# Performance work log

Measured on AMD Instinct MI355X. Metric: run time of the kernel, lower is better.

The kernel has to match this reference:

```python
import jax, jax.numpy as jnp
import numpy as np

HEADS, DIM_HEAD, BITS = 12, 64, 4


def quantize(q, bits):
    # per-tensor affine fake-quant, exactly as the torch quantize()
    s = (q.max() - q.min()) / (2.0 ** bits - 1.0)
    z = jnp.round(2.0 ** bits - 1.0 - q.max() / s)
    return jnp.round(q / s + z), s, z


def setup_inputs() -> dict:
    key = jax.random.key(0)
    k1, k2, k3, k4 = jax.random.split(key, 4)
    return {
        "x": jax.random.normal(k1, (4, 1024, 768), jnp.float32),
        "w_qkv": jax.random.normal(k2, (2304, 768), jnp.float32) * 0.02,  # torch Linear weight [out,in]
        "w_out": jax.random.normal(k3, (768, 768), jnp.float32) * 0.02,
        "b_out": jax.random.normal(k4, (768,), jnp.float32) * 0.02,
    }


def reference(x, w_qkv, w_out, b_out):
    scale = DIM_HEAD ** -0.5
    B, N, D = x.shape
    # --- quantized QKV projection: x @ W^T with zero-point correction ---
    xq, sx1, zx1 = quantize(x, BITS)
    w1, sw1, zw1 = quantize(w_qkv.T, BITS)  # [D, 3*inner]
    xqkv = (xq @ w1
            - w1.sum(0, keepdims=True) * zx1
            - xq.sum(2, keepdims=True) * zw1
            + zx1 * zw1 * D) * (sx1 * sw1)  # [B, N, 3*inner]
    q, k, v = jnp.split(xqkv, 3, axis=-1)
    to_heads = lambda t: t.reshape(B, N, HEADS, DIM_HEAD).transpose(0, 2, 1, 3)  # b h n d
    q, k, v = to_heads(q), to_heads(k), to_heads(v)
    # --- quantized QK^T (note: original omits the +zq*zk*d term) ---
    qq, sq, zq = quantize(q, BITS)
    kq, sk, zk = quantize(k.transpose(0, 1, 3, 2), BITS)  # b h d n
    dots = (qq @ kq
            - kq.sum(2, keepdims=True) * zq
            - qq.sum(3, keepdims=True) * zk) * (scale * sq * sk)  # b h n n
    a = jax.nn.softmax(dots, axis=-1)
    # --- quantized A @ V ---
    aq, sa, za = quantize(a, BITS)
    vq, sv, zv = quantize(v, BITS)
    out = (aq @ vq
           - vq.sum(2, keepdims=True) * za
           - aq.sum(3, keepdims=True) * zv
           + za * zv * N) * (sa * sv)  # b h n d
    out = out.transpose(0, 2, 1, 3).reshape(B, N, HEADS * DIM_HEAD)
    # --- quantized output projection (faithful to original: correction uses
    # xqkv.sum / xqkv width, reproducing the source's use of `x` here) ---
    oq, sx2, zx2 = quantize(out, BITS)
    w2, sw2, zw2 = quantize(w_out.T, BITS)  # [inner, D]
    o = (oq @ w2
         - w2.sum(0, keepdims=True) * zx2
         - xqkv.sum(2, keepdims=True) * zw2
         + zx2 * zw2 * xqkv.shape[2]) * (sx2 * sw2) + b_out
    return o
```

## Files before the change

kernel.cpp:

```cpp
#include <hip/hip_runtime.h>
#include <math.h>

#define HEADS 12
#define DH    64
#define Dm    768
#define I3    2304
#define Nn    1024
#define Mm    4096
#define BHt   48
#define LOG2E 1.4426950408889634f

#define P_X  0
#define P_W1 1
#define P_Q  2
#define P_K  3
#define P_V  4
#define P_A  5
#define P_O  6
#define P_W2 7

typedef int v4i __attribute__((ext_vector_type(4)));

#if __has_builtin(__builtin_amdgcn_exp2f)
#define EXP2(x) __builtin_amdgcn_exp2f(x)
#else
#define EXP2(x) exp2f(x)
#endif

__device__ inline unsigned encf(float f) {
    unsigned u = __float_as_uint(f);
    return (u & 0x80000000u) ? ~u : (u | 0x80000000u);
}
__device__ inline float decf(unsigned u) {
    return (u & 0x80000000u) ? __uint_as_float(u & 0x7fffffffu) : __uint_as_float(~u);
}
__device__ inline void get_sz(const unsigned* scal, int pair, float* s, float* z) {
    float mn = decf(scal[2 * pair]);
    float mx = decf(scal[2 * pair + 1]);
    float ss = (mx - mn) / 15.0f;
    *s = ss;
    *z = rintf(15.0f - mx / ss);
}

__device__ inline void swz_bh(int blk, int* bh, int* itile) {
    int xcd = blk & 7, idx = blk >> 3;
    *itile = idx & 15;
    *bh = xcd + 8 * (idx >> 4);
}

__global__ __launch_bounds__(256) void k_init(unsigned* scal, float* z1, int n1, float* z2, int n2) {
    int g = blockIdx.x * 256 + threadIdx.x;
    if (g < n1) z1[g] = 0.f;
    if (g < n2) z2[g] = 0.f;
    if (g < 8) { scal[2 * g] = 0xFFFFFFFFu; scal[2 * g + 1] = 0u; }
}

__global__ __launch_bounds__(256) void k_minmax3(const float* x, const float* w1, const float* w2,
                                                 unsigned* scal) {
    __shared__ float rmn[256], rmx[256];
    int bid = blockIdx.x, tid = threadIdx.x;
    const float* src; int rows, pair, b0, nb;
    if (bid < 256)      { src = x;  rows = 4096; pair = P_X;  b0 = 0;   nb = 256; }
    else if (bid < 384) { src = w1; rows = 2304; pair = P_W1; b0 = 256; nb = 128; }
    else                { src = w2; rows = 768;  pair = P_W2; b0 = 384; nb = 64;  }
    float mn = INFINITY, mx = -INFINITY;
    for (int r = bid - b0; r < rows; r += nb) {
        const float* row = src + (long)r * 768;
#pragma unroll
        for (int k = 0; k < 3; ++k) {
            float v = row[tid + k * 256];
            mn = fminf(mn, v); mx = fmaxf(mx, v);
        }
    }
    rmn[tid] = mn; rmx[tid] = mx; __syncthreads();
    for (int s = 128; s > 0; s >>= 1) {
        if (tid < s) { rmn[tid] = fminf(rmn[tid], rmn[tid + s]); rmx[tid] = fmaxf(rmx[tid], rmx[tid + s]); }
        __syncthreads();
    }
    if (tid == 0) {
        atomicMin(&scal[2 * pair], encf(rmn[0]));
        atomicMax(&scal[2 * pair + 1], encf(rmx[0]));
    }
}

__global__ __launch_bounds__(256) void k_quant3(const float* x, const float* w1, const float* w2,
                                                const unsigned* scal,
                                                signed char* xq, signed char* wq, signed char* w2q,
                                                float* rs_x, float* rs_w1, float* rs_w2) {
    __shared__ float red[256];
    int bid = blockIdx.x, tid = threadIdx.x;
    const float* src; signed char* dq; float* rs; int pair, r;
    if (bid < 4096)      { src = x;  dq = xq;  rs = rs_x;  pair = P_X;  r = bid; }
    else if (bid < 6400) { src = w1; dq = wq;  rs = rs_w1; pair = P_W1; r = bid - 4096; }
    else                 { src = w2; dq = w2q; rs = rs_w2; pair = P_W2; r = bid - 6400; }
    float s, z; get_sz(scal, pair, &s, &z);
    const float* row = src + (long)r * 768;
    signed char* drow = dq + (long)r * 768;
    float acc = 0.f;
#pragma unroll
    for (int k = 0; k < 3; ++k) {
        int c = tid + k * 256;
        float q = rintf(row[c] / s + z);
        drow[c] = (signed char)(int)q;
        acc += q;
    }
    red[tid] = acc; __syncthreads();
    for (int s2 = 128; s2 > 0; s2 >>= 1) { if (tid < s2) red[tid] += red[tid + s2]; __syncthreads(); }
    if (tid == 0) rs[r] = red[0];
}

__global__ __launch_bounds__(256) void k_quant_rows(const float* src, const unsigned* scal, int pair,
                                                    signed char* dq) {
    int r = blockIdx.x, tid = threadIdx.x;
    float s, z; get_sz(scal, pair, &s, &z);
    const float* row = src + (long)r * 768;
    signed char* drow = dq + (long)r * 768;
#pragma unroll
    for (int k = 0; k < 3; ++k) {
        int c = tid + k * 256;
        float q = rintf(row[c] / s + z);
        drow[c] = (signed char)(int)q;
    }
}

__global__ __launch_bounds__(256) void k_gemm_mfma(const signed char* A, const signed char* B,
                                                   const float* colsumB, const float* rowsumA,
                                                   const float* bias, float* C, int K, int ldC,
                                                   const unsigned* scal, int pairA, int pairB,
                                                   float corrK, int do_stats, float* rowsum_out,
                                                   unsigned* scal_mm) {
    __shared__ __align__(16) signed char As[128 * 64];
    __shared__ __align__(16) signed char Bs[128 * 64];
    __shared__ float red[256];
    int tid = threadIdx.x;
    int wave = tid >> 6, lane = tid & 63;
    int col16 = lane & 15, quad = lane >> 4;
    long rowbase = (long)blockIdx.y * 128;
    long colbase = (long)blockIdx.x * 128;

    int c4 = tid & 3, r4 = tid >> 2;
    const signed char* ag0 = A + (rowbase + r4) * K + c4 * 16;
    const signed char* ag1 = A + (rowbase + r4 + 64) * K + c4 * 16;
    const signed char* bg0 = B + (colbase + r4) * K + c4 * 16;
    const signed char* bg1 = B + (colbase + r4 + 64) * K + c4 * 16;
    int soff0 = ((r4 >> 4) << 10) + (c4 << 8) + ((r4 & 15) << 4);
    int soff1 = soff0 + 4096;

    v4i ra0 = *(const v4i*)ag0;
    v4i ra1 = *(const v4i*)ag1;
    v4i rb0 = *(const v4i*)bg0;
    v4i rb1 = *(const v4i*)bg1;

    const int afrag_off = wave * 2048 + quad * 256 + col16 * 16;
    const int bfrag_off = quad * 256 + col16 * 16;
    v4i acc[2][8] = {};
    int nk = K >> 6;
    for (int kt = 0; kt < nk; ++kt) {
        *(v4i*)(As + soff0) = ra0;
        *(v4i*)(As + soff1) = ra1;
        *(v4i*)(Bs + soff0) = rb0;
        *(v4i*)(Bs + soff1) = rb1;
        __syncthreads();
        if (kt + 1 < nk) {
            int ko = (kt + 1) << 6;
            ra0 = *(const v4i*)(ag0 + ko);
            ra1 = *(const v4i*)(ag1 + ko);
            rb0 = *(const v4i*)(bg0 + ko);
            rb1 = *(const v4i*)(bg1 + ko);
        }
        v4i af0 = *(const v4i*)(As + afrag_off);
        v4i af1 = *(const v4i*)(As + afrag_off + 1024);
        v4i bf[8];
#pragma unroll
        for (int g = 0; g < 8; ++g) bf[g] = *(const v4i*)(Bs + bfrag_off + g * 1024);
#pragma unroll
        for (int g = 0; g < 8; ++g) {
            acc[0][g] = __builtin_amdgcn_mfma_i32_16x16x64_i8(af0, bf[g], acc[0][g], 0, 0, 0);
            acc[1][g] = __builtin_amdgcn_mfma_i32_16x16x64_i8(af1, bf[g], acc[1][g], 0, 0, 0);
        }
        __syncthreads();
    }

    float sA, zA, sB, zB;
    get_sz(scal, pairA, &sA, &zA);
    get_sz(scal, pairB, &sB, &zB);
    float sAB = sA * sB;
    float zz = (zA * zB) * corrK;
    float vmn = INFINITY, vmx = -INFINITY;
    float rowpart[2][4] = {};
#pragma unroll
    for (int i2 = 0; i2 < 2; ++i2)
#pragma unroll
        for (int g = 0; g < 8; ++g) {
            long col = colbase + g * 16 + col16;
            float cs = colsumB[col] * zA;
            float bv = bias ? bias[col] : 0.f;
#pragma unroll
            for (int r = 0; r < 4; ++r) {
                long row = rowbase + wave * 32 + i2 * 16 + quad * 4 + r;
                float v = ((float)acc[i2][g][r] - cs - rowsumA[row] * zB + zz) * sAB + bv;
                C[row * ldC + col] = v;
                rowpart[i2][r] += v;
                vmn = fminf(vmn, v); vmx = fmaxf(vmx, v);
            }
        }
    if (do_stats) {
#pragma unroll
        for (int i2 = 0; i2 < 2; ++i2)
#pragma unroll
            for (int r = 0; r < 4; ++r) {
                float s = rowpart[i2][r];
                s += __shfl_xor(s, 1); s += __shfl_xor(s, 2);
                s += __shfl_xor(s, 4); s += __shfl_xor(s, 8);
                if (col16 == 0)
                    atomicAdd(&rowsum_out[rowbase + wave * 32 + i2 * 16 + quad * 4 + r], s);
            }
        int pair = P_Q + (int)(colbase / 768);
        red[tid] = vmx; __syncthreads();
        for (int s = 128; s > 0; s >>= 1) { if (tid < s) red[tid] = fmaxf(red[tid], red[tid + s]); __syncthreads(); }
        if (tid == 0) atomicMax(&scal_mm[2 * pair + 1], encf(red[0]));
        __syncthreads();
        red[tid] = vmn; __syncthreads();
        for (int s = 128; s > 0; s >>= 1) { if (tid < s) red[tid] = fminf(red[tid], red[tid + s]); __syncthreads(); }
        if (tid == 0) atomicMin(&scal_mm[2 * pair], encf(red[0]));
    }
}

__global__ __launch_bounds__(256) void k_quant_qkv2(const float* xqkv, const unsigned* scal,
                                                    signed char* qq, signed char* kq, signed char* vqT,
                                                    float* rowsum_qq, float* cskc, float* colsum_vq) {
    __shared__ __align__(16) signed char vt[64 * 80];
    __shared__ float vred[4][64];
    int blk = blockIdx.x;
    int bh = blk >> 4, itile = blk & 15;
    int tid = threadIdx.x;
    int wave = tid >> 6, d = tid & 63;
    int b = bh / HEADS, h = bh - HEADS * b;
    float sq, zq, sk, zk, sv, zv;
    get_sz(scal, P_Q, &sq, &zq);
    get_sz(scal, P_K, &sk, &zk);
    get_sz(scal, P_V, &sv, &zv);
    float zqcsc2 = zq * ((0.125f * sq) * sk) * LOG2E;
    int vb = 0;
    float vsum = 0.f;
    for (int ir = 0; ir < 16; ++ir) {
        int il = wave * 16 + ir;
        int i = itile * 64 + il;
        const float* row = xqkv + ((long)b * Nn + i) * I3 + h * DH;
        float q = rintf(row[d] / sq + zq);
        float k = rintf(row[768 + d] / sk + zk);
        float v = rintf(row[1536 + d] / sv + zv);
        long o = ((long)bh * Nn + i) * 64 + d;
        qq[o] = (signed char)(int)q;
        kq[o] = (signed char)(int)k;
        vsum += v;
        vb |= ((int)v & 0xff) << ((ir & 3) * 8);
        if ((ir & 3) == 3) {
            *(int*)(vt + d * 80 + (il & ~3)) = vb;
            vb = 0;
        }
        float s1 = q, s2 = k;
        for (int off = 32; off > 0; off >>= 1) {
            s1 += __shfl_down(s1, off);
            s2 += __shfl_down(s2, off);
        }
        if (d == 0) { rowsum_qq[bh * Nn + i] = s1; cskc[bh * Nn + i] = s2 * zqcsc2; }
    }
    vred[wave][d] = vsum;
    __syncthreads();
    int dd = tid >> 2, c = tid & 3;
    *(v4i*)(vqT + ((long)bh * 64 + dd) * 1024 + itile * 64 + c * 16) = *(const v4i*)(vt + dd * 80 + c * 16);
    if (tid < 64)
        atomicAdd(&colsum_vq[bh * 64 + tid],
                  ((vred[0][tid] + vred[1][tid]) + vred[2][tid]) + vred[3][tid]);
}

__global__ __launch_bounds__(256) void k_attn_a8(const signed char* qq, const signed char* kq,
                                                 const float* rowsum_qq, const float* cskc,
                                                 unsigned* scal, float* rowmax, float* sumexp) {
    __shared__ float red[256];
    int bh, itile;
    swz_bh(blockIdx.x, &bh, &itile);
    int tid = threadIdx.x;
    int wave = tid >> 6, lane = tid & 63;
    int col16 = lane & 15, quad = lane >> 4;
    int rowbase = itile * 64 + wave * 16;
    const signed char* kbase = kq + (long)bh * Nn * 64;
    const float* ck = cskc + bh * Nn;
    v4i afrag = *(const v4i*)(qq + ((long)bh * Nn + rowbase + col16) * 64 + quad * 16);
    float sq, zq, sk, zk;
    get_sz(scal, P_Q, &sq, &zq);
    get_sz(scal, P_K, &sk, &zk);
    float csc2 = ((0.125f * sq) * sk) * LOG2E;
    float rzc[4];
#pragma unroll
    for (int r = 0; r < 4; ++r)
        rzc[r] = rowsum_qq[bh * Nn + rowbase + quad * 4 + r] * zk * csc2;
    v4i zero = {0, 0, 0, 0};
    float m[4]    = {-INFINITY, -INFINITY, -INFINITY, -INFINITY};
    float se[4]   = {0.f, 0.f, 0.f, 0.f};
    float lmin[4] = {INFINITY, INFINITY, INFINITY, INFINITY};
    const signed char* kf = kbase + (long)col16 * 64 + quad * 16;
    const float* ckp = ck + col16;
    v4i kb[2][4];
    float ckc[4], ckn[4];
#pragma unroll
    for (int t = 0; t < 4; ++t) {
        kb[0][t] = *(const v4i*)(kf + (long)(t * 16) * 64);
        ckc[t] = ckp[t * 16];
    }
#pragma unroll 2
    for (int ch = 0; ch < 16; ++ch) {
        int cur = ch & 1, nxt = cur ^ 1;
        int pch = (ch < 15) ? ch + 1 : 15;
#pragma unroll
        for (int t = 0; t < 4; ++t) {
            kb[nxt][t] = *(const v4i*)(kf + (long)(pch * 64 + t * 16) * 64);
            ckn[t] = ckp[pch * 64 + t * 16];
        }
#pragma unroll
        for (int t = 0; t < 4; ++t) {
            v4i d = __builtin_amdgcn_mfma_i32_16x16x64_i8(afrag, kb[cur][t], zero, 0, 0, 0);
            float ckv = ckc[t];
#pragma unroll
            for (int r = 0; r < 4; ++r) {
                float dv = fmaf((float)d[r], csc2, -(ckv + rzc[r]));
                lmin[r] = fminf(lmin[r], dv);
                float mn = fmaxf(m[r], dv);
                float e = EXP2(fminf(m[r], dv) - mn);
                se[r] = (dv > m[r]) ? fmaf(se[r], e, 1.0f) : (se[r] + e);
                m[r] = mn;
            }
        }
#pragma unroll
        for (int t = 0; t < 4; ++t) ckc[t] = ckn[t];
    }
#pragma unroll
    for (int r = 0; r < 4; ++r) {
#pragma unroll
        for (int off = 1; off < 16; off <<= 1) {
            float mo = __shfl_xor(m[r], off);
            float so = __shfl_xor(se[r], off);
            float mino = __shfl_xor(lmin[r], off);
            float mn = fmaxf(m[r], mo);
            se[r] = fmaf(se[r], EXP2(m[r] - mn), so * EXP2(mo - mn));
            m[r] = mn;
            lmin[r] = fminf(lmin[r], mino);
        }
    }
    float amax_c = -INFINITY, amin_c = INFINITY;
    if (col16 == 0) {
#pragma unroll
        for (int r = 0; r < 4; ++r) {
            int grow = bh * Nn + rowbase + quad * 4 + r;
            rowmax[grow] = m[r];
            sumexp[grow] = se[r];
            amax_c = fmaxf(amax_c, 1.0f / se[r]);
            amin_c = fminf(amin_c, EXP2(lmin[r] - m[r]) / se[r]);
        }
    }
    red[tid] = amax_c; __syncthreads();
    for (int s = 128; s > 0; s >>= 1) { if (tid < s) red[tid] = fmaxf(red[tid], red[tid + s]); __syncthreads(); }
    if (tid == 0) atomicMax(&scal[2 * P_A + 1], encf(red[0]));
    __syncthreads();
    red[tid] = amin_c; __syncthreads();
    for (int s = 128; s > 0; s >>= 1) { if (tid < s) red[tid] = fminf(red[tid], red[tid + s]); __syncthreads(); }
    if (tid == 0) atomicMin(&scal[2 * P_A], encf(red[0]));
}

__global__ __launch_bounds__(256) void k_attn_b8(const signed char* qq, const signed char* kq,
                                                 const signed char* vqT, const float* rowsum_qq,
                                                 const float* cskc, const float* colsum_vq,
                                                 const float* rowmax, const float* sumexp,
                                                 unsigned* scal, float* out_mat) {
    __shared__ __align__(16) signed char AqB[8192];
    __shared__ float red[256];
    int bh, itile;
    swz_bh(blockIdx.x, &bh, &itile);
    int tid = threadIdx.x;
    int wave = tid >> 6, lane = tid & 63;
    int col16 = lane & 15, quad = lane >> 4;
    int rowbase = itile * 64 + wave * 16;
    int b = bh / HEADS, h = bh - HEADS * b;
    const signed char* kbase = kq + (long)bh * Nn * 64;
    const signed char* vbase = vqT + (long)bh * 64 * 1024;
    const float* ck = cskc + bh * Nn;
    v4i afrag = *(const v4i*)(qq + ((long)bh * Nn + rowbase + col16) * 64 + quad * 16);
    float sq, zq, sk, zk, sv, zv, sa, za;
    get_sz(scal, P_Q, &sq, &zq);
    get_sz(scal, P_K, &sk, &zk);
    get_sz(scal, P_V, &sv, &zv);
    get_sz(scal, P_A, &sa, &za);
    float csc2 = ((0.125f * sq) * sk) * LOG2E;
    float roff[4], crcp[4];
#pragma unroll
    for (int r = 0; r < 4; ++r) {
        int row = bh * Nn + rowbase + quad * 4 + r;
        roff[r] = rowsum_qq[row] * zk * csc2 + rowmax[row];
        crcp[r] = 1.0f / (sumexp[row] * sa);
    }
    v4i accPV[4] = {};
    float rs_a[4] = {0.f, 0.f, 0.f, 0.f};
    v4i zero = {0, 0, 0, 0};
    const signed char* kf = kbase + (long)col16 * 64 + quad * 16;
    const float* ckp = ck + col16;
    const int pa_off = wave * 1024 + col16 * 64 + ((quad ^ (col16 >> 2)) << 4);

    v4i kb0[4], kb1[4];
    float ckr0[4], ckr1[4];
#pragma unroll
    for (int t = 0; t < 4; ++t) {
        kb0[t] = *(const v4i*)(kf + (long)(t * 16) * 64);
        ckr0[t] = ckp[t * 16];
        kb1[t] = *(const v4i*)(kf + (long)(64 + t * 16) * 64);
        ckr1[t] = ckp[64 + t * 16];
    }

#define QUANT_CHUNK(BUF, KB, CKR)                                                       \
    {                                                                                   \
        signed char* myAq = AqB + (BUF) * 4096 + wave * 1024;                           \
        _Pragma("unroll")                                                               \
        for (int t = 0; t < 4; ++t) {                                                   \
            v4i d = __builtin_amdgcn_mfma_i32_16x16x64_i8(afrag, KB[t], zero, 0, 0, 0); \
            float ckv = CKR[t];                                                         \
            int cswz = ((t ^ quad) << 4) + col16;                                       \
            _Pragma("unroll")                                                           \
            for (int r = 0; r < 4; ++r) {                                               \
                float es = fmaf((float)d[r], csc2, -(ckv + roff[r]));                   \
                float fastv = fmaf(EXP2(es), crcp[r], za);                              \
                float aqv = rintf(fastv);                                               \
                rs_a[r] += aqv;                                                         \
                myAq[(quad * 4 + r) * 64 + cswz] = (signed char)(int)aqv;               \
            }                                                                           \
        }                                                                               \
    }

#define BODY(CH, CUR, KBc, CKc, KBn, CKn)                                               \
    {                                                                                   \
        v4i pa = *(const v4i*)(AqB + (CUR) * 4096 + pa_off);                            \
        v4i bv[4];                                                                      \
        _Pragma("unroll")                                                               \
        for (int g = 0; g < 4; ++g)                                                     \
            bv[g] = *(const v4i*)(vbase + (long)(g * 16 + col16) * 1024 + (CH) * 64 + quad * 16); \
        if ((CH) < 14) {                                                                \
            _Pragma("unroll")                                                           \
            for (int t = 0; t < 4; ++t) {                                               \
                KBc[t] = *(const v4i*)(kf + (long)(((CH) + 2) * 64 + t * 16) * 64);     \
                CKc[t] = ckp[((CH) + 2) * 64 + t * 16];                                 \
            }                                                                           \
        }                                                                               \
        if ((CH) < 15) QUANT_CHUNK(1 - (CUR), KBn, CKn)                                 \
        _Pragma("unroll")                                                               \
        for (int g = 0; g < 4; ++g)                                                     \
            accPV[g] = __builtin_amdgcn_mfma_i32_16x16x64_i8(pa, bv[g], accPV[g], 0, 0, 0); \
    }

    QUANT_CHUNK(0, kb0, ckr0)
    for (int ch2 = 0; ch2 < 8; ++ch2) {
        int ch = ch2 * 2;
        BODY(ch, 0, kb0, ckr0, kb1, ckr1)
        BODY(ch + 1, 1, kb1, ckr1, kb0, ckr0)
    }
#undef BODY
#undef QUANT_CHUNK

#pragma unroll
    for (int r = 0; r < 4; ++r)
        for (int off = 1; off < 16; off <<= 1) rs_a[r] += __shfl_xor(rs_a[r], off);
    float sav = sa * sv;
    float zz = (za * zv) * 1024.0f;
    float vmn = INFINITY, vmx = -INFINITY;
#pragma unroll
    for (int g = 0; g < 4; ++g) {
        int d = g * 16 + col16;
        float cs = colsum_vq[bh * 64 + d] * za;
#pragma unroll
        for (int r = 0; r < 4; ++r) {
            int i = rowbase + quad * 4 + r;
            float v = ((float)accPV[g][r] - cs - rs_a[r] * zv + zz) * sav;
            out_mat[((long)b * Nn + i) * Dm + h * DH + d] = v;
            vmn = fminf(vmn, v); vmx = fmaxf(vmx, v);
        }
    }
    red[tid] = vmx; __syncthreads();
    for (int s = 128; s > 0; s >>= 1) { if (tid < s) red[tid] = fmaxf(red[tid], red[tid + s]); __syncthreads(); }
    if (tid == 0) atomicMax(&scal[2 * P_O + 1], encf(red[0]));
    __syncthreads();
    red[tid] = vmn; __syncthreads();
    for (int s = 128; s > 0; s >>= 1) { if (tid < s) red[tid] = fminf(red[tid], red[tid + s]); __syncthreads(); }
    if (tid == 0) atomicMin(&scal[2 * P_O], encf(red[0]));
}

extern "C" void kernel_launch(void* const* d_in, const int* in_sizes, int n_in,
                              void* d_out, int out_size, void* d_ws, size_t ws_size,
                              hipStream_t stream) {
    const float* x     = (const float*)d_in[0];
    const float* w_qkv = (const float*)d_in[1];
    const float* w_out = (const float*)d_in[2];
    const float* b_out = (const float*)d_in[3];

    char* ws = (char*)d_ws;
    size_t off = 0;
    auto alloc = [&](size_t n) -> char* {
        char* p = ws + off;
        off = (off + n + 255) & ~(size_t)255;
        return p;
    };
    unsigned*    scal        = (unsigned*)alloc(64);
    float*       xqkv        = (float*)alloc((size_t)Mm * I3 * 4);
    float*       out_mat     = (float*)alloc((size_t)Mm * Dm * 4);
    signed char* xq          = (signed char*)alloc((size_t)Mm * Dm);
    signed char* wq          = (signed char*)alloc((size_t)I3 * Dm);
    signed char* w2q         = (signed char*)alloc((size_t)Dm * Dm);
    signed char* oq          = (signed char*)alloc((size_t)Mm * Dm);
    signed char* qq          = (signed char*)alloc((size_t)BHt * Nn * DH);
    signed char* kq          = (signed char*)alloc((size_t)BHt * Nn * DH);
    signed char* vqT         = (signed char*)alloc((size_t)BHt * Nn * DH);
    float*       rowsum_xq   = (float*)alloc((size_t)Mm * 4);
    float*       colsum_w1   = (float*)alloc((size_t)I3 * 4);
    float*       colsum_w2   = (float*)alloc((size_t)Dm * 4);
    float*       rowsum_xqkv = (float*)alloc((size_t)Mm * 4);
    float*       rowsum_qq   = (float*)alloc((size_t)BHt * Nn * 4);
    float*       cskc        = (float*)alloc((size_t)BHt * Nn * 4);
    float*       colsum_vq   = (float*)alloc((size_t)BHt * DH * 4);
    float*       rowmax      = (float*)alloc((size_t)BHt * Nn * 4);
    float*       sumexp      = (float*)alloc((size_t)BHt * Nn * 4);

    k_init<<<28, 256, 0, stream>>>(scal, rowsum_xqkv, Mm, colsum_vq, BHt * DH);

    k_minmax3<<<448, 256, 0, stream>>>(x, w_qkv, w_out, scal);
    k_quant3<<<7168, 256, 0, stream>>>(x, w_qkv, w_out, scal, xq, wq, w2q,
                                       rowsum_xq, colsum_w1, colsum_w2);

    {
        dim3 g(I3 / 128, Mm / 128);
        k_gemm_mfma<<<g, 256, 0, stream>>>(xq, wq, colsum_w1, rowsum_xq, nullptr, xqkv,
                                           Dm, I3, scal, P_X, P_W1, 768.0f,
                                           1, rowsum_xqkv, scal);
    }

    k_quant_qkv2<<<BHt * 16, 256, 0, stream>>>(xqkv, scal, qq, kq, vqT,
                                               rowsum_qq, cskc, colsum_vq);

    k_attn_a8<<<BHt * 16, 256, 0, stream>>>(qq, kq, rowsum_qq, cskc, scal, rowmax, sumexp);
    k_attn_b8<<<BHt * 16, 256, 0, stream>>>(qq, kq, vqT, rowsum_qq, cskc, colsum_vq,
                                            rowmax, sumexp, scal, out_mat);

    k_quant_rows<<<Mm, 256, 0, stream>>>(out_mat, scal, P_O, oq);

    {
        dim3 g(Dm / 128, Mm / 128);
        k_gemm_mfma<<<g, 256, 0, stream>>>(oq, w2q, colsum_w2, rowsum_xqkv, b_out, (float*)d_out,
                                           Dm, Dm, scal, P_O, P_W2, 2304.0f,
                                           0, nullptr, nullptr);
    }
}
```

Before: 256.3 us.

## Transpose MFMA operands in attention kernels so each lane owns one query row

Swaps the A/B operand order of the int8 MFMA in both attention passes, so each lane's accumulator holds four key columns for a single query row rather than four rows. Row statistics (max, sum-exp, min, rowsum of quantized A) then reduce across 4 quads instead of 16 lanes. Column corrections become vectorized float4 loads. Quantized probabilities are packed into 32-bit LDS writes, and the output is written as float4. The aim is fewer shuffles, fewer scalar byte stores and loads, and fewer prefetch registers, at the cost of reworking the LDS layout for the PV operand.

```diff
diff --git a/kernel.cpp b/kernel.cpp
--- a/kernel.cpp
+++ b/kernel.cpp
@@ -19,7 +19,8 @@
 #define P_O  6
 #define P_W2 7
 
-typedef int v4i __attribute__((ext_vector_type(4)));
+typedef int   v4i __attribute__((ext_vector_type(4)));
+typedef float v4f __attribute__((ext_vector_type(4)));
 
 #if __has_builtin(__builtin_amdgcn_exp2f)
 #define EXP2(x) __builtin_amdgcn_exp2f(x)
@@ -286,45 +287,37 @@
     int col16 = lane & 15, quad = lane >> 4;
     int rowbase = itile * 64 + wave * 16;
     const signed char* kbase = kq + (long)bh * Nn * 64;
-    const float* ck = cskc + bh * Nn;
-    v4i afrag = *(const v4i*)(qq + ((long)bh * Nn + rowbase + col16) * 64 + quad * 16);
+    v4i qfrag = *(const v4i*)(qq + ((long)bh * Nn + rowbase + col16) * 64 + quad * 16);
     float sq, zq, sk, zk;
     get_sz(scal, P_Q, &sq, &zq);
     get_sz(scal, P_K, &sk, &zk);
     float csc2 = ((0.125f * sq) * sk) * LOG2E;
-    float rzc[4];
-#pragma unroll
-    for (int r = 0; r < 4; ++r)
-        rzc[r] = rowsum_qq[bh * Nn + rowbase + quad * 4 + r] * zk * csc2;
+    int irow = bh * Nn + rowbase + col16;
+    float roff = rowsum_qq[irow] * zk * csc2;
     v4i zero = {0, 0, 0, 0};
     float m[4]    = {-INFINITY, -INFINITY, -INFINITY, -INFINITY};
     float se[4]   = {0.f, 0.f, 0.f, 0.f};
     float lmin[4] = {INFINITY, INFINITY, INFINITY, INFINITY};
     const signed char* kf = kbase + (long)col16 * 64 + quad * 16;
-    const float* ckp = ck + col16;
+    const float* ckq = cskc + bh * Nn + quad * 4;
     v4i kb[2][4];
-    float ckc[4], ckn[4];
-#pragma unroll
-    for (int t = 0; t < 4; ++t) {
+#pragma unroll
+    for (int t = 0; t < 4; ++t)
         kb[0][t] = *(const v4i*)(kf + (long)(t * 16) * 64);
-        ckc[t] = ckp[t * 16];
-    }
 #pragma unroll 2
     for (int ch = 0; ch < 16; ++ch) {
         int cur = ch & 1, nxt = cur ^ 1;
         int pch = (ch < 15) ? ch + 1 : 15;
 #pragma unroll
-        for (int t = 0; t < 4; ++t) {
+        for (int t = 0; t < 4; ++t)
             kb[nxt][t] = *(const v4i*)(kf + (long)(pch * 64 + t * 16) * 64);
-            ckn[t] = ckp[pch * 64 + t * 16];
-        }
-#pragma unroll
-        for (int t = 0; t < 4; ++t) {
-            v4i d = __builtin_amdgcn_mfma_i32_16x16x64_i8(afrag, kb[cur][t], zero, 0, 0, 0);
-            float ckv = ckc[t];
+#pragma unroll
+        for (int s = 0; s < 4; ++s) {
+            v4i d = __builtin_amdgcn_mfma_i32_16x16x64_i8(kb[cur][s], qfrag, zero, 0, 0, 0);
+            v4f ck4 = *(const v4f*)(ckq + ch * 64 + s * 16);
 #pragma unroll
             for (int r = 0; r < 4; ++r) {
-                float dv = fmaf((float)d[r], csc2, -(ckv + rzc[r]));
+                float dv = fmaf((float)d[r], csc2, -(ck4[r] + roff));
                 lmin[r] = fminf(lmin[r], dv);
                 float mn = fmaxf(m[r], dv);
                 float e = EXP2(fminf(m[r], dv) - mn);
@@ -332,33 +325,28 @@
                 m[r] = mn;
             }
         }
-#pragma unroll
-        for (int t = 0; t < 4; ++t) ckc[t] = ckn[t];
-    }
-#pragma unroll
-    for (int r = 0; r < 4; ++r) {
-#pragma unroll
-        for (int off = 1; off < 16; off <<= 1) {
-            float mo = __shfl_xor(m[r], off);
-            float so = __shfl_xor(se[r], off);
-            float mino = __shfl_xor(lmin[r], off);
-            float mn = fmaxf(m[r], mo);
-            se[r] = fmaf(se[r], EXP2(m[r] - mn), so * EXP2(mo - mn));
-            m[r] = mn;
-            lmin[r] = fminf(lmin[r], mino);
-        }
-    }
-    float amax_c = -INFINITY, amin_c = INFINITY;
-    if (col16 == 0) {
-#pragma unroll
-        for (int r = 0; r < 4; ++r) {
-            int grow = bh * Nn + rowbase + quad * 4 + r;
-            rowmax[grow] = m[r];
-            sumexp[grow] = se[r];
-            amax_c = fmaxf(amax_c, 1.0f / se[r]);
-            amin_c = fminf(amin_c, EXP2(lmin[r] - m[r]) / se[r]);
-        }
-    }
+    }
+    float mm = fmaxf(fmaxf(m[0], m[1]), fmaxf(m[2], m[3]));
+    float seT = fmaf(se[0], EXP2(m[0] - mm),
+               fmaf(se[1], EXP2(m[1] - mm),
+               fmaf(se[2], EXP2(m[2] - mm), se[3] * EXP2(m[3] - mm))));
+    float lmT = fminf(fminf(lmin[0], lmin[1]), fminf(lmin[2], lmin[3]));
+#pragma unroll
+    for (int off = 16; off <= 32; off <<= 1) {
+        float mo = __shfl_xor(mm, off);
+        float so = __shfl_xor(seT, off);
+        float lo = __shfl_xor(lmT, off);
+        float mn = fmaxf(mm, mo);
+        seT = fmaf(seT, EXP2(mm - mn), so * EXP2(mo - mn));
+        mm = mn;
+        lmT = fminf(lmT, lo);
+    }
+    if (quad == 0) {
+        rowmax[irow] = mm;
+        sumexp[irow] = seT;
+    }
+    float amax_c = 1.0f / seT;
+    float amin_c = EXP2(lmT - mm) / seT;
     red[tid] = amax_c; __syncthreads();
     for (int s = 128; s > 0; s >>= 1) { if (tid < s) red[tid] = fmaxf(red[tid], red[tid + s]); __syncthreads(); }
     if (tid == 0) atomicMax(&scal[2 * P_A + 1], encf(red[0]));
@@ -384,103 +372,95 @@
     int b = bh / HEADS, h = bh - HEADS * b;
     const signed char* kbase = kq + (long)bh * Nn * 64;
     const signed char* vbase = vqT + (long)bh * 64 * 1024;
-    const float* ck = cskc + bh * Nn;
-    v4i afrag = *(const v4i*)(qq + ((long)bh * Nn + rowbase + col16) * 64 + quad * 16);
+    v4i qfrag = *(const v4i*)(qq + ((long)bh * Nn + rowbase + col16) * 64 + quad * 16);
     float sq, zq, sk, zk, sv, zv, sa, za;
     get_sz(scal, P_Q, &sq, &zq);
     get_sz(scal, P_K, &sk, &zk);
     get_sz(scal, P_V, &sv, &zv);
     get_sz(scal, P_A, &sa, &za);
     float csc2 = ((0.125f * sq) * sk) * LOG2E;
-    float roff[4], crcp[4];
-#pragma unroll
-    for (int r = 0; r < 4; ++r) {
-        int row = bh * Nn + rowbase + quad * 4 + r;
-        roff[r] = rowsum_qq[row] * zk * csc2 + rowmax[row];
-        crcp[r] = 1.0f / (sumexp[row] * sa);
-    }
+    int irow = bh * Nn + rowbase + col16;
+    float roff = rowsum_qq[irow] * zk * csc2 + rowmax[irow];
+    float crcp = 1.0f / (sumexp[irow] * sa);
     v4i accPV[4] = {};
-    float rs_a[4] = {0.f, 0.f, 0.f, 0.f};
+    float rs_a = 0.f;
     v4i zero = {0, 0, 0, 0};
     const signed char* kf = kbase + (long)col16 * 64 + quad * 16;
-    const float* ckp = ck + col16;
-    const int pa_off = wave * 1024 + col16 * 64 + ((quad ^ (col16 >> 2)) << 4);
+    const float* ckq = cskc + bh * Nn + quad * 4;
+    const int wbase = wave * 1024 + col16 * 16 + quad * 4;
+    const int rbase = wave * 1024 + quad * 256 + col16 * 16;
 
     v4i kb0[4], kb1[4];
-    float ckr0[4], ckr1[4];
 #pragma unroll
     for (int t = 0; t < 4; ++t) {
         kb0[t] = *(const v4i*)(kf + (long)(t * 16) * 64);
-        ckr0[t] = ckp[t * 16];
         kb1[t] = *(const v4i*)(kf + (long)(64 + t * 16) * 64);
-        ckr1[t] = ckp[64 + t * 16];
-    }
-
-#define QUANT_CHUNK(BUF, KB, CKR)                                                       \
+    }
+
+#define QUANT_CHUNK(CH, BUF, KB)                                                        \
     {                                                                                   \
-        signed char* myAq = AqB + (BUF) * 4096 + wave * 1024;                           \
         _Pragma("unroll")                                                               \
-        for (int t = 0; t < 4; ++t) {                                                   \
-            v4i d = __builtin_amdgcn_mfma_i32_16x16x64_i8(afrag, KB[t], zero, 0, 0, 0); \
-            float ckv = CKR[t];                                                         \
-            int cswz = ((t ^ quad) << 4) + col16;                                       \
+        for (int s = 0; s < 4; ++s) {                                                   \
+            v4i d = __builtin_amdgcn_mfma_i32_16x16x64_i8(KB[s], qfrag, zero, 0, 0, 0); \
+            v4f ck4 = *(const v4f*)(ckq + (CH) * 64 + s * 16);                          \
+            unsigned pks = 0;                                                           \
             _Pragma("unroll")                                                           \
             for (int r = 0; r < 4; ++r) {                                               \
-                float es = fmaf((float)d[r], csc2, -(ckv + roff[r]));                   \
-                float fastv = fmaf(EXP2(es), crcp[r], za);                              \
-                float aqv = rintf(fastv);                                               \
-                rs_a[r] += aqv;                                                         \
-                myAq[(quad * 4 + r) * 64 + cswz] = (signed char)(int)aqv;               \
+                float es = fmaf((float)d[r], csc2, -(ck4[r] + roff));                   \
+                float aqv = rintf(fmaf(EXP2(es), crcp, za));                            \
+                rs_a += aqv;                                                            \
+                pks |= ((unsigned)(int)aqv & 255u) << (8 * r);                          \
             }                                                                           \
+            *(int*)(AqB + (BUF) * 4096 + wbase + s * 256) = (int)pks;                   \
         }                                                                               \
     }
 
-#define BODY(CH, CUR, KBc, CKc, KBn, CKn)                                               \
+#define BODY(CH, CUR, KBc, KBn)                                                         \
     {                                                                                   \
-        v4i pa = *(const v4i*)(AqB + (CUR) * 4096 + pa_off);                            \
+        v4i pa = *(const v4i*)(AqB + (CUR) * 4096 + rbase);                             \
         v4i bv[4];                                                                      \
         _Pragma("unroll")                                                               \
         for (int g = 0; g < 4; ++g)                                                     \
             bv[g] = *(const v4i*)(vbase + (long)(g * 16 + col16) * 1024 + (CH) * 64 + quad * 16); \
         if ((CH) < 14) {                                                                \
             _Pragma("unroll")                                                           \
-            for (int t = 0; t < 4; ++t) {                                               \
+            for (int t = 0; t < 4; ++t)                                                 \
                 KBc[t] = *(const v4i*)(kf + (long)(((CH) + 2) * 64 + t * 16) * 64);     \
-                CKc[t] = ckp[((CH) + 2) * 64 + t * 16];                                 \
-            }                                                                           \
         }                                                                               \
-        if ((CH) < 15) QUANT_CHUNK(1 - (CUR), KBn, CKn)                                 \
+        if ((CH) < 15) QUANT_CHUNK((CH) + 1, 1 - (CUR), KBn)                            \
         _Pragma("unroll")                                                               \
         for (int g = 0; g < 4; ++g)                                                     \
-            accPV[g] = __builtin_amdgcn_mfma_i32_16x16x64_i8(pa, bv[g], accPV[g], 0, 0, 0); \
-    }
-
-    QUANT_CHUNK(0, kb0, ckr0)
+            accPV[g] = __builtin_amdgcn_mfma_i32_16x16x64_i8(bv[g], pa, accPV[g], 0, 0, 0); \
+    }
+
+    QUANT_CHUNK(0, 0, kb0)
     for (int ch2 = 0; ch2 < 8; ++ch2) {
         int ch = ch2 * 2;
-        BODY(ch, 0, kb0, ckr0, kb1, ckr1)
-        BODY(ch + 1, 1, kb1, ckr1, kb0, ckr0)
+        BODY(ch, 0, kb0, kb1)
+        BODY(ch + 1, 1, kb1, kb0)
     }
 #undef BODY
 #undef QUANT_CHUNK
 
-#pragma unroll
-    for (int r = 0; r < 4; ++r)
-        for (int off = 1; off < 16; off <<= 1) rs_a[r] += __shfl_xor(rs_a[r], off);
+    rs_a += __shfl_xor(rs_a, 16);
+    rs_a += __shfl_xor(rs_a, 32);
+
     float sav = sa * sv;
     float zz = (za * zv) * 1024.0f;
     float vmn = INFINITY, vmx = -INFINITY;
+    long obase = ((long)b * Nn + rowbase + col16) * Dm + h * DH;
 #pragma unroll
     for (int g = 0; g < 4; ++g) {
-        int d = g * 16 + col16;
-        float cs = colsum_vq[bh * 64 + d] * za;
-#pragma unroll
-        for (int r = 0; r < 4; ++r) {
-            int i = rowbase + quad * 4 + r;
-            float v = ((float)accPV[g][r] - cs - rs_a[r] * zv + zz) * sav;
-            out_mat[((long)b * Nn + i) * Dm + h * DH + d] = v;
+        int d4 = g * 16 + quad * 4;
+        v4f cs4 = *(const v4f*)(colsum_vq + bh * 64 + d4);
+        v4f ov;
+#pragma unroll
+        for (int rr = 0; rr < 4; ++rr) {
+            float v = ((float)accPV[g][rr] - cs4[rr] * za - rs_a * zv + zz) * sav;
+            ov[rr] = v;
             vmn = fminf(vmn, v); vmx = fmaxf(vmx, v);
         }
+        *(v4f*)(out_mat + obase + d4) = ov;
     }
     red[tid] = vmx; __syncthreads();
     for (int s = 128; s > 0; s >>= 1) { if (tid < s) red[tid] = fmaxf(red[tid], red[tid + s]); __syncthreads(); }
```

New measurement: 261.6 us. +2.1%, slower.
